# Kernel optimization log

Measured on AMD Instinct MI355X. Metric: run time of the kernel, lower is better.

The kernel has to match this reference:

```python
import jax, jax.numpy as jnp
import numpy as np

SIGMA = 1.0  # GaussianKernel slope


def setup_inputs() -> dict:
    key = jax.random.key(0)
    ks = jax.random.split(key, 6)
    B, F, E = 2048, 65536, 128
    return {
        "rel": jax.random.normal(ks[0], (B, E), dtype=jnp.float32),
        "arg1": jax.random.normal(ks[1], (B, E), dtype=jnp.float32),
        "arg2": jax.random.normal(ks[2], (B, E), dtype=jnp.float32),
        "fact_rel": jax.random.normal(ks[3], (F, E), dtype=jnp.float32),
        "fact_arg1": jax.random.normal(ks[4], (F, E), dtype=jnp.float32),
        "fact_arg2": jax.random.normal(ks[5], (F, E), dtype=jnp.float32),
    }


def reference(rel, arg1, arg2, fact_rel, fact_arg1, fact_arg2):
    # query: [B, 3E], facts: [F, 3E]  (concat scoring)
    query = jnp.concatenate([rel, arg1, arg2], axis=1)
    facts = jnp.concatenate([fact_rel, fact_arg1, fact_arg2], axis=1)
    # Gaussian kernel: exp(-||q - f||^2 / (2*sigma^2)), via ||q||^2 - 2 q.f + ||f||^2
    q_sq = jnp.sum(query * query, axis=1, keepdims=True)          # [B, 1]
    f_sq = jnp.sum(facts * facts, axis=1)                          # [F]
    d2 = q_sq - 2.0 * jnp.einsum('bd,fd->bf', query, facts) + f_sq[None, :]
    d2 = jnp.maximum(d2, 0.0)  # numerical guard for squared distance
    scores = jnp.exp(-d2 / (2.0 * SIGMA * SIGMA))                  # [B, F]
    return jnp.max(scores, axis=1)                                 # [B]
```

## Files before the change

### kernel.cpp

```cpp
#include <hip/hip_runtime.h>


typedef __attribute__((ext_vector_type(4))) float f32x4;
typedef __attribute__((ext_vector_type(2))) long lx2;
typedef __attribute__((ext_vector_type(4))) long lx4;
typedef __attribute__((ext_vector_type(8))) int i32x8;
typedef __attribute__((ext_vector_type(8))) __bf16 bf16x8;
typedef __attribute__((ext_vector_type(4))) unsigned short us4;

#define AS1 __attribute__((address_space(1)))
#define AS3 __attribute__((address_space(3)))
__device__ __forceinline__ void gl2lds16(const void* g, void* l) {
    __builtin_amdgcn_global_load_lds((const AS1 unsigned int*)g,
                                     (AS3 unsigned int*)l, 16, 0, 0);
}

__device__ __forceinline__ unsigned char f2e4m3(float x) {
    unsigned int u = __float_as_uint(x);
    unsigned int sign = (u >> 24) & 0x80u;
    unsigned int a = u & 0x7fffffffu;
    if (a >= 0x43e00000u) return (unsigned char)(sign | 0x7e);
    if (a < 0x3c800000u) {
        int m = (int)rintf(__uint_as_float(a) * 512.0f);
        return (unsigned char)(sign | (unsigned)m);
    }
    unsigned int base = a - 0x3c000000u;
    unsigned int lsb = (base >> 20) & 1u;
    unsigned int code = (base + 0x7ffffu + lsb) >> 20;
    return (unsigned char)(sign | code);
}

__device__ __forceinline__ unsigned short f2bf(float f) {
    unsigned int u = __float_as_uint(f);
    u = (u + 0x7fffu + ((u >> 16) & 1u)) >> 16;
    return (unsigned short)u;
}

__device__ __forceinline__ void conv_row_fp8(const float* __restrict__ p0,
                                             const float* __restrict__ p1,
                                             const float* __restrict__ p2,
                                             int row, unsigned char* __restrict__ outb,
                                             float* __restrict__ sq) {
    const int lane = threadIdx.x & 63;
    float s = 0.f;
    if (lane < 48) {
        const int p = lane >> 4;
        const int off = (lane & 15) * 8;
        const float* src = ((p == 0) ? p0 : (p == 1) ? p1 : p2) + (size_t)row * 128 + off;
        const float4 v0 = *(const float4*)(src);
        const float4 v1 = *(const float4*)(src + 4);
        s = v0.x * v0.x + v0.y * v0.y + v0.z * v0.z + v0.w * v0.w +
            v1.x * v1.x + v1.y * v1.y + v1.z * v1.z + v1.w * v1.w;
        const int k = p * 128 + off;
        const int g = k >> 6;
        const int ss = (k >> 5) & 1;
        const int quad = (k >> 3) & 3;
        const int cs = quad ^ ((row >> 1) & 3);
        unsigned long long pk =
            (unsigned long long)f2e4m3(v0.x)        | ((unsigned long long)f2e4m3(v0.y) << 8) |
            ((unsigned long long)f2e4m3(v0.z) << 16) | ((unsigned long long)f2e4m3(v0.w) << 24) |
            ((unsigned long long)f2e4m3(v1.x) << 32) | ((unsigned long long)f2e4m3(v1.y) << 40) |
            ((unsigned long long)f2e4m3(v1.z) << 48) | ((unsigned long long)f2e4m3(v1.w) << 56);
        *(unsigned long long*)(outb + (size_t)row * 384 + g * 64 + cs * 16 + ss * 8) = pk;
    }
#pragma unroll
    for (int off = 32; off >= 1; off >>= 1) s += __shfl_xor(s, off, 64);
    if (lane == 0) sq[row] = s;
}

__global__ void prep_kernel(const float* __restrict__ rel, const float* __restrict__ a1,
                            const float* __restrict__ a2, const float* __restrict__ fr,
                            const float* __restrict__ fa1, const float* __restrict__ fa2,
                            unsigned char* __restrict__ Qf, unsigned char* __restrict__ Ff,
                            float* __restrict__ qsq, float* __restrict__ fsq,
                            unsigned int* __restrict__ outbits, int B, int F) {
    const int wave = (int)(threadIdx.x >> 6);
    const int nq = B / 4;
    if ((int)blockIdx.x < nq) {
        conv_row_fp8(rel, a1, a2, blockIdx.x * 4 + wave, Qf, qsq);
        if (blockIdx.x == 0)
            for (int i = threadIdx.x; i < B; i += 256) outbits[i] = 0x7f800000u;
    } else {
        const int row = ((int)blockIdx.x - nq) * 4 + wave;
        if (row < F) conv_row_fp8(fr, fa1, fa2, row, Ff, fsq);
    }
}

__device__ __forceinline__ void stage_tile(const unsigned char* __restrict__ Ff,
                                           unsigned char* buf, int n0, int tid) {
#pragma unroll
    for (int it = 0; it < 6; ++it) {
        int iid = it * 256 + tid;
        gl2lds16(Ff + (size_t)(n0 + ((iid >> 2) & 63)) * 384 +
                     (iid >> 9) * 128 + ((iid >> 8) & 1) * 64 + (iid & 3) * 16,
                 buf + (size_t)iid * 16);
    }
}

__global__ __launch_bounds__(256, 2)
void gemm_dbuf_kernel(const unsigned char* __restrict__ Qf,
                      const unsigned char* __restrict__ Ff,
                      const float* __restrict__ qsq, const float* __restrict__ fsq,
                      unsigned int* __restrict__ outbits, int ntiles) {
    __shared__ __align__(16) unsigned char Bs[2][24576];

    const int tid = threadIdx.x;
    const int lane = tid & 63;
    const int wid = tid >> 6;
    const int col = lane & 15, quad = lane >> 4;
    const int swc = ((col >> 1) & 3);
    const int cp = (quad ^ swc) * 16;
    const int m0 = blockIdx.y * 256;
    const int nbase = blockIdx.x * (ntiles * 64);
    const int SCL = 0x7f;

    union pk_t { lx4 l; i32x8 i; };

    i32x8 af8[4][3];
#pragma unroll
    for (int i = 0; i < 4; ++i) {
        const unsigned char* base = Qf + (size_t)(m0 + wid * 64 + i * 16 + col) * 384;
#pragma unroll
        for (int kk = 0; kk < 3; ++kk) {
            lx2 t0 = *(const lx2*)(base + kk * 128 + cp);
            lx2 t1 = *(const lx2*)(base + kk * 128 + 64 + cp);
            pk_t p; p.l.x = t0.x; p.l.y = t0.y; p.l.z = t1.x; p.l.w = t1.y;
            af8[i][kk] = p.i;
        }
    }

    float rowmin[16];
#pragma unroll
    for (int v = 0; v < 16; ++v) rowmin[v] = 3.0e38f;

    stage_tile(Ff, Bs[0], nbase, tid);
    for (int t = 0; t < ntiles; ++t) {
        __syncthreads();
        if (t + 1 < ntiles) stage_tile(Ff, Bs[(t + 1) & 1], nbase + (t + 1) * 64, tid);
        const unsigned char* bb = Bs[t & 1];
        const int n0 = nbase + t * 64;

        f32x4 acc[4][4];
#pragma unroll
        for (int j = 0; j < 4; ++j) {
            float seed = -0.5f * fsq[n0 + j * 16 + col];
            f32x4 z = {seed, seed, seed, seed};
#pragma unroll
            for (int i = 0; i < 4; ++i) acc[i][j] = z;
        }
#pragma unroll
        for (int j = 0; j < 4; ++j) {
#pragma unroll
            for (int kk = 0; kk < 3; ++kk) {
                const unsigned char* pb = bb + kk * 8192 + (j * 16 + col) * 64 + cp;
                lx2 t0 = *(const lx2*)(pb);
                lx2 t1 = *(const lx2*)(pb + 4096);
                pk_t p; p.l.x = t0.x; p.l.y = t0.y; p.l.z = t1.x; p.l.w = t1.y;
                i32x8 bv8 = p.i;
#pragma unroll
                for (int i = 0; i < 4; ++i)
                    acc[i][j] = __builtin_amdgcn_mfma_scale_f32_16x16x128_f8f6f4(
                        af8[i][kk], bv8, acc[i][j], 0, 0, 0, SCL, 0, SCL);
            }
        }
#pragma unroll
        for (int i = 0; i < 4; ++i)
#pragma unroll
            for (int r = 0; r < 4; ++r) {
                float mn = rowmin[i * 4 + r];
#pragma unroll
                for (int j = 0; j < 4; ++j)
                    mn = fminf(mn, -2.0f * acc[i][j][r]);
                rowmin[i * 4 + r] = mn;
            }
    }

#pragma unroll
    for (int v = 0; v < 16; ++v) {
        float mn = rowmin[v];
#pragma unroll
        for (int off = 1; off < 16; off <<= 1) mn = fminf(mn, __shfl_xor(mn, off, 64));
        rowmin[v] = mn;
    }
    if (col == 0) {
#pragma unroll
        for (int i = 0; i < 4; ++i)
#pragma unroll
            for (int r = 0; r < 4; ++r) {
                const int row = m0 + wid * 64 + i * 16 + quad * 4 + r;
                float d2 = fmaxf(qsq[row] + rowmin[i * 4 + r], 0.0f);
                atomicMin(outbits + row, __float_as_uint(d2));
            }
    }
}

__global__ void finalize_kernel(float* out, int n) {
    int i = blockIdx.x * blockDim.x + threadIdx.x;
    if (i < n) {
        float d2 = __uint_as_float(((unsigned int*)out)[i]);
        out[i] = expf(-0.5f * d2);
    }
}

__global__ void init_min_kernel(unsigned int* ob, int n) {
    int i = blockIdx.x * blockDim.x + threadIdx.x;
    if (i < n) ob[i] = 0x7f800000u;
}

__global__ void conv_rows_kernel(const float* __restrict__ p0, const float* __restrict__ p1,
                                 const float* __restrict__ p2, unsigned short* __restrict__ outb,
                                 float* __restrict__ sq, int nrows) {
    const int lane = threadIdx.x & 63;
    const int wave = threadIdx.x >> 6;
    const int row = blockIdx.x * 4 + wave;
    if (row >= nrows) return;
    float s = 0.f;
#pragma unroll
    for (int c = 0; c < 6; ++c) {
        int k = c * 64 + lane;
        const float* src = (k < 128) ? p0 : (k < 256) ? p1 : p2;
        float v = src[(size_t)row * 128 + (k & 127)];
        s += v * v;
        if (outb) outb[(size_t)row * 384 + k] = f2bf(v);
    }
#pragma unroll
    for (int off = 32; off >= 1; off >>= 1) s += __shfl_xor(s, off, 64);
    if (lane == 0) sq[row] = s;
}

__global__ __launch_bounds__(256)
void gemm_lean_kernel(const unsigned short* __restrict__ Qb,
                      const float* __restrict__ f0, const float* __restrict__ f1,
                      const float* __restrict__ f2,
                      const float* __restrict__ qsq, const float* __restrict__ fsq,
                      unsigned int* __restrict__ outbits, int K) {
    __shared__ __align__(16) unsigned short As[128 * 32];
    __shared__ __align__(16) unsigned short Bs[128 * 32];
    __shared__ float smin[128 * 2];

    const int tid = threadIdx.x;
    const int lane = tid & 63;
    const int wid = tid >> 6;
    const int wm = wid >> 1, wn = wid & 1;
    const int col = lane & 15, quad = lane >> 4;
    const int m0 = blockIdx.x * 128;
    const int n0 = blockIdx.y * 128;

    f32x4 acc[4][4];
#pragma unroll
    for (int i = 0; i < 4; ++i)
#pragma unroll
        for (int j = 0; j < 4; ++j) {
            f32x4 z = {0.f, 0.f, 0.f, 0.f};
            acc[i][j] = z;
        }

    const int nk = K >> 5;
    for (int kk = 0; kk < nk; ++kk) {
        const int k0 = kk << 5;
        __syncthreads();
#pragma unroll
        for (int it = 0; it < 2; ++it) {
            int iid = it * 256 + tid;
            int row = iid >> 2, ch = iid & 3;
            gl2lds16(Qb + ((size_t)(m0 + row) * K + k0 + ch * 8), As + (row * 32 + ch * 8));
        }
        const float* src = (k0 < 128) ? f0 : (k0 < 256) ? f1 : f2;
        const int kp = k0 & 127;
#pragma unroll
        for (int it = 0; it < 4; ++it) {
            int iid = it * 256 + tid;
            int row = iid >> 3, ch = iid & 7;
            const float4 v = *(const float4*)(src + (size_t)(n0 + row) * 128 + kp + ch * 4);
            us4 w = {f2bf(v.x), f2bf(v.y), f2bf(v.z), f2bf(v.w)};
            *(us4*)(Bs + (row * 32 + ch * 4)) = w;
        }
        __syncthreads();

        bf16x8 afr[4], bfv[4];
#pragma unroll
        for (int i = 0; i < 4; ++i)
            afr[i] = *(const bf16x8*)(As + ((wm * 64 + i * 16 + col) * 32 + quad * 8));
#pragma unroll
        for (int j = 0; j < 4; ++j)
            bfv[j] = *(const bf16x8*)(Bs + ((wn * 64 + j * 16 + col) * 32 + quad * 8));
#pragma unroll
        for (int i = 0; i < 4; ++i)
#pragma unroll
            for (int j = 0; j < 4; ++j)
                acc[i][j] = __builtin_amdgcn_mfma_f32_16x16x32_bf16(afr[i], bfv[j], acc[i][j], 0, 0, 0);
    }

    float fs[4];
#pragma unroll
    for (int j = 0; j < 4; ++j) fs[j] = fsq[n0 + wn * 64 + j * 16 + col];
#pragma unroll
    for (int i = 0; i < 4; ++i) {
#pragma unroll
        for (int r = 0; r < 4; ++r) {
            const int mrow = wm * 64 + i * 16 + quad * 4 + r;
            const float qs = qsq[m0 + mrow];
            float mn = 3.0e38f;
#pragma unroll
            for (int j = 0; j < 4; ++j) {
                float d2 = qs + fs[j] - 2.0f * acc[i][j][r];
                mn = fminf(mn, fmaxf(d2, 0.0f));
            }
#pragma unroll
            for (int off = 1; off < 16; off <<= 1) mn = fminf(mn, __shfl_xor(mn, off, 64));
            if (col == 0) smin[mrow * 2 + wn] = mn;
        }
    }
    __syncthreads();
    if (tid < 128) {
        float v = fminf(smin[tid * 2 + 0], smin[tid * 2 + 1]);
        atomicMin(outbits + m0 + tid, __float_as_uint(v));
    }
}

__global__ __launch_bounds__(256)
void tier3_kernel(const float* __restrict__ rel, const float* __restrict__ a1,
                  const float* __restrict__ a2, const float* __restrict__ fr,
                  const float* __restrict__ fa1, const float* __restrict__ fa2,
                  unsigned int* __restrict__ outbits) {
    __shared__ float qs[16][384];
    __shared__ float red[4][16];
    const int tid = threadIdx.x;
    const int qbase = blockIdx.y * 16;
    const int fbase = blockIdx.x * 2048;
    for (int i = tid; i < 16 * 384; i += 256) {
        int r = i / 384, c = i % 384;
        const float* src = (c < 128) ? rel : (c < 256) ? a1 : a2;
        qs[r][c] = src[(size_t)(qbase + r) * 128 + (c & 127)];
    }
    __syncthreads();
    float mn[16];
#pragma unroll
    for (int q = 0; q < 16; ++q) mn[q] = 3.0e38f;
    for (int fi = 0; fi < 2048; fi += 256) {
        const int f = fbase + fi + tid;
        float acc[16];
#pragma unroll
        for (int q = 0; q < 16; ++q) acc[q] = 0.f;
#pragma unroll
        for (int p = 0; p < 3; ++p) {
            const float* fptr = ((p == 0) ? fr : (p == 1) ? fa1 : fa2) + (size_t)f * 128;
            for (int k4 = 0; k4 < 32; ++k4) {
                const float4 fv = *(const float4*)(fptr + k4 * 4);
#pragma unroll
                for (int q = 0; q < 16; ++q) {
                    float d0 = fv.x - qs[q][p * 128 + k4 * 4 + 0];
                    float d1 = fv.y - qs[q][p * 128 + k4 * 4 + 1];
                    float d2 = fv.z - qs[q][p * 128 + k4 * 4 + 2];
                    float d3 = fv.w - qs[q][p * 128 + k4 * 4 + 3];
                    acc[q] += d0 * d0 + d1 * d1 + d2 * d2 + d3 * d3;
                }
            }
        }
#pragma unroll
        for (int q = 0; q < 16; ++q) mn[q] = fminf(mn[q], fmaxf(acc[q], 0.f));
    }
#pragma unroll
    for (int q = 0; q < 16; ++q) {
        float v = mn[q];
#pragma unroll
        for (int off = 32; off >= 1; off >>= 1) v = fminf(v, __shfl_xor(v, off, 64));
        if ((tid & 63) == 0) red[tid >> 6][q] = v;
    }
    __syncthreads();
    if (tid < 16) {
        float v = fminf(fminf(red[0][tid], red[1][tid]), fminf(red[2][tid], red[3][tid]));
        atomicMin(outbits + qbase + tid, __float_as_uint(v));
    }
}

extern "C" void kernel_launch(void* const* d_in, const int* in_sizes, int n_in,
                              void* d_out, int out_size, void* d_ws, size_t ws_size,
                              hipStream_t stream) {
    const float* rel = (const float*)d_in[0];
    const float* a1 = (const float*)d_in[1];
    const float* a2 = (const float*)d_in[2];
    const float* fr = (const float*)d_in[3];
    const float* fa1 = (const float*)d_in[4];
    const float* fa2 = (const float*)d_in[5];

    const int E = 128, K = 384;
    const int B = in_sizes[0] / E;
    const int F = in_sizes[3] / E;

    float* out = (float*)d_out;
    unsigned int* outbits = (unsigned int*)d_out;

    const size_t ff_bytes = (size_t)F * K;
    const size_t qf_bytes = (size_t)B * K;
    const size_t need_full = ff_bytes + qf_bytes + (size_t)F * 4 + (size_t)B * 4;
    const size_t qb_bytes = (size_t)B * K * 2;
    const size_t need_lean = qb_bytes + (size_t)F * 4 + (size_t)B * 4;

    const bool shapes_ok = (B % 256 == 0) && (F % 1024 == 0);
    if (ws_size >= need_full && shapes_ok) {
        unsigned char* Ff = (unsigned char*)d_ws;
        unsigned char* Qf = (unsigned char*)d_ws + ff_bytes;
        float* fsq = (float*)((char*)d_ws + ff_bytes + qf_bytes);
        float* qsq = fsq + F;
        prep_kernel<<<B / 4 + F / 4, 256, 0, stream>>>(rel, a1, a2, fr, fa1, fa2,
                                                       Qf, Ff, qsq, fsq, outbits, B, F);
        gemm_dbuf_kernel<<<dim3(F / 1024, B / 256), 256, 0, stream>>>(
            Qf, Ff, qsq, fsq, outbits, 16);
    } else if (ws_size >= need_lean && B % 128 == 0 && F % 128 == 0) {
        unsigned short* Qb = (unsigned short*)d_ws;
        float* fsq = (float*)((char*)d_ws + qb_bytes);
        float* qsq = fsq + F;
        init_min_kernel<<<(B + 255) / 256, 256, 0, stream>>>(outbits, B);
        conv_rows_kernel<<<B / 4, 256, 0, stream>>>(rel, a1, a2, Qb, qsq, B);
        conv_rows_kernel<<<F / 4, 256, 0, stream>>>(fr, fa1, fa2, nullptr, fsq, F);
        gemm_lean_kernel<<<dim3(B / 128, F / 128), 256, 0, stream>>>(
            Qb, fr, fa1, fa2, qsq, fsq, outbits, K);
    } else {
        init_min_kernel<<<(B + 255) / 256, 256, 0, stream>>>(outbits, B);
        tier3_kernel<<<dim3(F / 2048, B / 16), 256, 0, stream>>>(rel, a1, a2, fr, fa1, fa2, outbits);
    }

    finalize_kernel<<<(B + 255) / 256, 256, 0, stream>>>(out, B);
}
```

Measured before the change: 175.8 us.

## Halve per-block M tile to raise occupancy and prefetch fsq per tile

Each block now covers 128 query rows instead of 256, with every wave owning 32 rows. This cuts accumulator and A-fragment registers and raises the launch bound to 3 blocks per CU, giving more occupancy and twice as many blocks. Each block still streams the same fact tiles, so total LDS staging traffic for facts doubles. The fsq values for the next tile are loaded alongside the tile staging, and the row reduction tracks a max of the accumulator, folding the -2 scale into the final fma.

```diff
diff --git a/kernel.cpp b/kernel.cpp
--- a/kernel.cpp
+++ b/kernel.cpp
@@ -97,11 +97,11 @@
     }
 }
 
-__global__ __launch_bounds__(256, 2)
-void gemm_dbuf_kernel(const unsigned char* __restrict__ Qf,
-                      const unsigned char* __restrict__ Ff,
-                      const float* __restrict__ qsq, const float* __restrict__ fsq,
-                      unsigned int* __restrict__ outbits, int ntiles) {
+__global__ __launch_bounds__(256, 3)
+void gemm_w32_kernel(const unsigned char* __restrict__ Qf,
+                     const unsigned char* __restrict__ Ff,
+                     const float* __restrict__ qsq, const float* __restrict__ fsq,
+                     unsigned int* __restrict__ outbits, int ntiles) {
     __shared__ __align__(16) unsigned char Bs[2][24576];
 
     const int tid = threadIdx.x;
@@ -110,16 +110,16 @@
     const int col = lane & 15, quad = lane >> 4;
     const int swc = ((col >> 1) & 3);
     const int cp = (quad ^ swc) * 16;
-    const int m0 = blockIdx.y * 256;
+    const int m0 = blockIdx.y * 128;
     const int nbase = blockIdx.x * (ntiles * 64);
     const int SCL = 0x7f;
 
     union pk_t { lx4 l; i32x8 i; };
 
-    i32x8 af8[4][3];
-#pragma unroll
-    for (int i = 0; i < 4; ++i) {
-        const unsigned char* base = Qf + (size_t)(m0 + wid * 64 + i * 16 + col) * 384;
+    i32x8 af8[2][3];
+#pragma unroll
+    for (int i = 0; i < 2; ++i) {
+        const unsigned char* base = Qf + (size_t)(m0 + wid * 32 + i * 16 + col) * 384;
 #pragma unroll
         for (int kk = 0; kk < 3; ++kk) {
             lx2 t0 = *(const lx2*)(base + kk * 128 + cp);
@@ -129,24 +129,32 @@
         }
     }
 
-    float rowmin[16];
-#pragma unroll
-    for (int v = 0; v < 16; ++v) rowmin[v] = 3.0e38f;
+    float rowmax[8];
+#pragma unroll
+    for (int v = 0; v < 8; ++v) rowmax[v] = -3.0e38f;
+
+    float fs_cur[4], fs_nxt[4];
+#pragma unroll
+    for (int j = 0; j < 4; ++j) fs_cur[j] = fsq[nbase + j * 16 + col];
 
     stage_tile(Ff, Bs[0], nbase, tid);
     for (int t = 0; t < ntiles; ++t) {
         __syncthreads();
-        if (t + 1 < ntiles) stage_tile(Ff, Bs[(t + 1) & 1], nbase + (t + 1) * 64, tid);
+        if (t + 1 < ntiles) {
+            stage_tile(Ff, Bs[(t + 1) & 1], nbase + (t + 1) * 64, tid);
+#pragma unroll
+            for (int j = 0; j < 4; ++j)
+                fs_nxt[j] = fsq[nbase + (t + 1) * 64 + j * 16 + col];
+        }
         const unsigned char* bb = Bs[t & 1];
-        const int n0 = nbase + t * 64;
-
-        f32x4 acc[4][4];
+
+        f32x4 acc[2][4];
 #pragma unroll
         for (int j = 0; j < 4; ++j) {
-            float seed = -0.5f * fsq[n0 + j * 16 + col];
+            float seed = -0.5f * fs_cur[j];
             f32x4 z = {seed, seed, seed, seed};
 #pragma unroll
-            for (int i = 0; i < 4; ++i) acc[i][j] = z;
+            for (int i = 0; i < 2; ++i) acc[i][j] = z;
         }
 #pragma unroll
         for (int j = 0; j < 4; ++j) {
@@ -158,37 +166,39 @@
                 pk_t p; p.l.x = t0.x; p.l.y = t0.y; p.l.z = t1.x; p.l.w = t1.y;
                 i32x8 bv8 = p.i;
 #pragma unroll
-                for (int i = 0; i < 4; ++i)
+                for (int i = 0; i < 2; ++i)
                     acc[i][j] = __builtin_amdgcn_mfma_scale_f32_16x16x128_f8f6f4(
                         af8[i][kk], bv8, acc[i][j], 0, 0, 0, SCL, 0, SCL);
             }
         }
 #pragma unroll
-        for (int i = 0; i < 4; ++i)
+        for (int i = 0; i < 2; ++i)
 #pragma unroll
             for (int r = 0; r < 4; ++r) {
-                float mn = rowmin[i * 4 + r];
+                float mx = rowmax[i * 4 + r];
 #pragma unroll
                 for (int j = 0; j < 4; ++j)
-                    mn = fminf(mn, -2.0f * acc[i][j][r]);
-                rowmin[i * 4 + r] = mn;
+                    mx = fmaxf(mx, acc[i][j][r]);
+                rowmax[i * 4 + r] = mx;
             }
-    }
-
-#pragma unroll
-    for (int v = 0; v < 16; ++v) {
-        float mn = rowmin[v];
-#pragma unroll
-        for (int off = 1; off < 16; off <<= 1) mn = fminf(mn, __shfl_xor(mn, off, 64));
-        rowmin[v] = mn;
+#pragma unroll
+        for (int j = 0; j < 4; ++j) fs_cur[j] = fs_nxt[j];
+    }
+
+#pragma unroll
+    for (int v = 0; v < 8; ++v) {
+        float mx = rowmax[v];
+#pragma unroll
+        for (int off = 1; off < 16; off <<= 1) mx = fmaxf(mx, __shfl_xor(mx, off, 64));
+        rowmax[v] = mx;
     }
     if (col == 0) {
 #pragma unroll
-        for (int i = 0; i < 4; ++i)
+        for (int i = 0; i < 2; ++i)
 #pragma unroll
             for (int r = 0; r < 4; ++r) {
-                const int row = m0 + wid * 64 + i * 16 + quad * 4 + r;
-                float d2 = fmaxf(qsq[row] + rowmin[i * 4 + r], 0.0f);
+                const int row = m0 + wid * 32 + i * 16 + quad * 4 + r;
+                float d2 = fmaxf(fmaf(-2.0f, rowmax[i * 4 + r], qsq[row]), 0.0f);
                 atomicMin(outbits + row, __float_as_uint(d2));
             }
     }
@@ -397,7 +407,7 @@
     const size_t qb_bytes = (size_t)B * K * 2;
     const size_t need_lean = qb_bytes + (size_t)F * 4 + (size_t)B * 4;
 
-    const bool shapes_ok = (B % 256 == 0) && (F % 1024 == 0);
+    const bool shapes_ok = (B % 128 == 0) && (F % 1024 == 0);
     if (ws_size >= need_full && shapes_ok) {
         unsigned char* Ff = (unsigned char*)d_ws;
         unsigned char* Qf = (unsigned char*)d_ws + ff_bytes;
@@ -405,7 +415,7 @@
         float* qsq = fsq + F;
         prep_kernel<<<B / 4 + F / 4, 256, 0, stream>>>(rel, a1, a2, fr, fa1, fa2,
                                                        Qf, Ff, qsq, fsq, outbits, B, F);
-        gemm_dbuf_kernel<<<dim3(F / 1024, B / 256), 256, 0, stream>>>(
+        gemm_w32_kernel<<<dim3(F / 1024, B / 128), 256, 0, stream>>>(
             Qf, Ff, qsq, fsq, outbits, 16);
     } else if (ws_size >= need_lean && B % 128 == 0 && F % 128 == 0) {
         unsigned short* Qb = (unsigned short*)d_ws;
```

After: 181.0 us. 1.03x slower.
